# Optimization experiments

Hardware: AMD Instinct MI355X
Metric: run time of the kernel (lower is better)

## Reference

```python
import jax, jax.numpy as jnp
import numpy as np

SIGMA = np.float32(np.pi)  # Gaussian envelope std used by the Gabor synthesis


def gabor_filters(theta, lam, h, w):
    """Generate [G, h, w] Gabor filters from orientation theta and frequency lam."""
    ys = jnp.arange(h, dtype=jnp.float32) - (h - 1) / 2.0  # centered grid
    xs = jnp.arange(w, dtype=jnp.float32) - (w - 1) / 2.0
    y, x = jnp.meshgrid(ys, xs, indexing='ij')  # [h, w]
    th = theta[:, None, None]  # [G,1,1]
    l = lam[:, None, None]
    xr = x * jnp.cos(th) + y * jnp.sin(th)    # rotated coords [G,h,w]
    yr = -x * jnp.sin(th) + y * jnp.cos(th)
    env = jnp.exp(-(xr ** 2 + yr ** 2) / (2.0 * SIGMA ** 2))
    return env * jnp.cos(2.0 * jnp.float32(np.pi) * xr * l)  # [G,h,w]


def setup_inputs() -> dict:
    key = jax.random.key(0)
    k1, k2 = jax.random.split(key)
    no_g = 4
    co, ci, h, w = 512, 512, 9, 9
    x = jax.random.normal(k1, (co, ci, h, w), dtype=jnp.float32)
    theta = jnp.arange(no_g, dtype=jnp.float32) / no_g * jnp.float32(np.pi)
    lam = jax.random.uniform(k2, (no_g,), dtype=jnp.float32,
                             minval=-1.0 / np.sqrt(no_g), maxval=1.0 / np.sqrt(no_g))
    return {"x": x, "theta": theta, "lam": lam}


def reference(x, theta, lam):
    # x: [C_out, C_in, kH, kW] conv weight; theta/lam: [no_g]
    G = theta.shape[0]
    co, ci, h, w = x.shape
    g = gabor_filters(theta, lam, h, w)              # [G, h, w]
    out = g[:, None, None, :, :] * x[None]           # [G, co, ci, h, w]
    return out.reshape(G * co, ci, h, w)             # view(-1, *out.size()[2:])
```

## Files before the change

kernel.cpp:

```cpp
#include <hip/hip_runtime.h>
#include <math.h>

#define NG   4
#define HW   81
#define NELT (512 * 512 * 81)
#define N4   (NELT / 4)
#define BLK  256
#define NBLK (N4 / BLK)

__global__ __launch_bounds__(BLK) void gabor_mul_kernel(
    const float* __restrict__ x,
    const float* __restrict__ theta,
    const float* __restrict__ lam,
    float* __restrict__ out)
{
    __shared__ float gf[NG * HW];

    const float PI_F = 3.14159274101257324f;
    const float INV_2SIG2 = 1.0f / (2.0f * PI_F * PI_F);
    for (int t = threadIdx.x; t < NG * HW; t += BLK) {
        int gi = t / HW;
        int p  = t - gi * HW;
        int i  = p / 9;
        int j  = p - i * 9;
        float fy = (float)(i - 4);
        float fx = (float)(j - 4);
        float th = theta[gi];
        float l  = lam[gi];
        float c  = cosf(th);
        float s  = sinf(th);
        float xr  = fx * c + fy * s;
        float env = expf(-(fx * fx + fy * fy) * INV_2SIG2);
        gf[t] = env * cosf(2.0f * PI_F * xr * l);
    }
    __syncthreads();

    unsigned tid  = blockIdx.x * BLK + threadIdx.x;
    unsigned base = tid * 4u;
    unsigned p0   = base % 81u;
    unsigned p1 = p0 + 1u; if (p1 >= 81u) p1 -= 81u;
    unsigned p2 = p1 + 1u; if (p2 >= 81u) p2 -= 81u;
    unsigned p3 = p2 + 1u; if (p3 >= 81u) p3 -= 81u;

    const float4 xv = ((const float4*)x)[tid];

    float4* out4 = (float4*)out;
#pragma unroll
    for (int gi = 0; gi < NG; ++gi) {
        const float* gr = &gf[gi * HW];
        float4 o;
        o.x = xv.x * gr[p0];
        o.y = xv.y * gr[p1];
        o.z = xv.z * gr[p2];
        o.w = xv.w * gr[p3];
        out4[(size_t)gi * (size_t)N4 + (size_t)tid] = o;
    }
}

extern "C" void kernel_launch(void* const* d_in, const int* in_sizes, int n_in,
                              void* d_out, int out_size, void* d_ws, size_t ws_size,
                              hipStream_t stream) {
    const float* x     = (const float*)d_in[0];
    const float* theta = (const float*)d_in[1];
    const float* lam   = (const float*)d_in[2];
    float* out = (float*)d_out;

    gabor_mul_kernel<<<NBLK, BLK, 0, stream>>>(x, theta, lam, out);
}
```

Measured before the change: 391.1 us.

## Use grid-stride loop, interleaved LDS filter layout, and nontemporal output stores

The launch drops from one block per 1024 elements to a fixed 2048-block grid with a grid-stride loop, so the per-block filter setup is amortized over many iterations. Filters are stored as one float4 per spatial position holding all four orientations, so each element needs four vector LDS reads instead of sixteen scalar ones. Output writes use nontemporal stores to reduce cache pollution on this write-heavy kernel. The fixed grid size may leave fewer waves in flight to hide memory latency.

After: 393.9 us. About the same (+0.7%).

```diff
diff --git a/kernel.cpp b/kernel.cpp
--- a/kernel.cpp
+++ b/kernel.cpp
@@ -6,7 +6,10 @@
 #define NELT (512 * 512 * 81)
 #define N4   (NELT / 4)
 #define BLK  256
-#define NBLK (N4 / BLK)
+#define NBLK 2048
+#define NTHR (NBLK * BLK)
+
+typedef float v4f __attribute__((ext_vector_type(4)));
 
 __global__ __launch_bounds__(BLK) void gabor_mul_kernel(
     const float* __restrict__ x,
@@ -14,46 +17,55 @@
     const float* __restrict__ lam,
     float* __restrict__ out)
 {
-    __shared__ float gf[NG * HW];
+    __shared__ v4f gf4[HW];
 
     const float PI_F = 3.14159274101257324f;
     const float INV_2SIG2 = 1.0f / (2.0f * PI_F * PI_F);
-    for (int t = threadIdx.x; t < NG * HW; t += BLK) {
-        int gi = t / HW;
-        int p  = t - gi * HW;
-        int i  = p / 9;
-        int j  = p - i * 9;
+    if (threadIdx.x < HW) {
+        int p = threadIdx.x;
+        int i = p / 9;
+        int j = p - i * 9;
         float fy = (float)(i - 4);
         float fx = (float)(j - 4);
-        float th = theta[gi];
-        float l  = lam[gi];
-        float c  = cosf(th);
-        float s  = sinf(th);
-        float xr  = fx * c + fy * s;
         float env = expf(-(fx * fx + fy * fy) * INV_2SIG2);
-        gf[t] = env * cosf(2.0f * PI_F * xr * l);
+        v4f v;
+#pragma unroll
+        for (int g = 0; g < NG; ++g) {
+            float th = theta[g];
+            float l  = lam[g];
+            float xr = fx * cosf(th) + fy * sinf(th);
+            v[g] = env * cosf(2.0f * PI_F * xr * l);
+        }
+        gf4[p] = v;
     }
     __syncthreads();
 
-    unsigned tid  = blockIdx.x * BLK + threadIdx.x;
-    unsigned base = tid * 4u;
-    unsigned p0   = base % 81u;
-    unsigned p1 = p0 + 1u; if (p1 >= 81u) p1 -= 81u;
-    unsigned p2 = p1 + 1u; if (p2 >= 81u) p2 -= 81u;
-    unsigned p3 = p2 + 1u; if (p3 >= 81u) p3 -= 81u;
+    const v4f* __restrict__ x4 = (const v4f*)x;
+    v4f* out4 = (v4f*)out;
 
-    const float4 xv = ((const float4*)x)[tid];
+    unsigned gtid = blockIdx.x * BLK + threadIdx.x;
+    for (unsigned u = gtid; u < N4; u += NTHR) {
+        unsigned base = u * 4u;
+        unsigned p0 = base % 81u;
+        unsigned p1 = p0 + 1u; if (p1 >= 81u) p1 -= 81u;
+        unsigned p2 = p1 + 1u; if (p2 >= 81u) p2 -= 81u;
+        unsigned p3 = p2 + 1u; if (p3 >= 81u) p3 -= 81u;
 
-    float4* out4 = (float4*)out;
+        const v4f xv = x4[u];
+        const v4f g0 = gf4[p0];
+        const v4f g1 = gf4[p1];
+        const v4f g2 = gf4[p2];
+        const v4f g3 = gf4[p3];
+
 #pragma unroll
-    for (int gi = 0; gi < NG; ++gi) {
-        const float* gr = &gf[gi * HW];
-        float4 o;
-        o.x = xv.x * gr[p0];
-        o.y = xv.y * gr[p1];
-        o.z = xv.z * gr[p2];
-        o.w = xv.w * gr[p3];
-        out4[(size_t)gi * (size_t)N4 + (size_t)tid] = o;
+        for (int g = 0; g < NG; ++g) {
+            v4f o;
+            o.x = xv.x * g0[g];
+            o.y = xv.y * g1[g];
+            o.z = xv.z * g2[g];
+            o.w = xv.w * g3[g];
+            __builtin_nontemporal_store(o, &out4[(size_t)g * (size_t)N4 + (size_t)u]);
+        }
     }
 }
 
```
